# Performance work log

Hardware: AMD Instinct MI355X
Metric: run time of the kernel (lower is better)

## Reference

```python
import jax, jax.numpy as jnp
import numpy as np

EPS = 1e-12  # torch F.normalize clamp epsilon
NOISE = np.array([1e-05, 2e-05, 3e-05], dtype=np.float32)  # diagonal regularizer


def setup_inputs() -> dict:
    key = jax.random.key(0)
    B, C = 65536, 128
    v_feat = jax.random.normal(key, (B, C, 3), dtype=jnp.float32)
    return {"v_feat": v_feat}


def reference(v_feat):
    # L2 normalize each 3-vector (B, C, 3) along last dim
    norm = jnp.sqrt(jnp.sum(v_feat * v_feat, axis=-1, keepdims=True))
    v = v_feat / jnp.maximum(norm, EPS)

    # Covariance M = v^T v  -> (B, 3, 3), plus tiny diagonal noise for stability
    M = jnp.einsum('bci,bcj->bij', v, v) + jnp.diag(jnp.asarray(NOISE))[None, :, :]

    # Batched symmetric 3x3 eigendecomposition (ascending eigenvalues)
    _, evecs = jnp.linalg.eigh(M)  # evecs: (B, 3, 3), columns are eigenvectors
    v1 = evecs[:, :, 0]  # (B, 3)
    v2 = evecs[:, :, 1]

    # Sign disambiguation: align with the mean direction of the features
    def fix_sign(vec):
        s = jnp.sign(jnp.sum(v * vec[:, None, :], axis=(1, 2)))  # (B,)
        s = jnp.where(s == 0, 1.0, s)
        return vec * s[:, None]

    v1 = fix_sign(v1)
    v2 = fix_sign(v2)
    v3 = jnp.cross(v1, v2)

    # Frame: columns [v1 v2 v3] -> (B, 3, 3)
    return jnp.stack([v1, v2, v3], axis=-1)
```

## Files before the change

### kernel.cpp

```cpp
#include <hip/hip_runtime.h>
#include <math.h>
#include <stdint.h>


#define WAVES_PER_BLOCK 4
#define BLOCK (WAVES_PER_BLOCK * 64)
#define ITERS 2
#define BATCHES_PER_WAVE (4 * ITERS)
#define BPB (WAVES_PER_BLOCK * BATCHES_PER_WAVE)

template <int CTRL>
__device__ __forceinline__ float ror16_f32(float v) {
    union { float f; int i; } u, r;
    u.f = v;
    r.i = __builtin_amdgcn_mov_dpp(u.i, CTRL, 0xF, 0xF, true);
    return r.f;
}

__device__ __forceinline__ double fast_rsqrt2(double x) {
    double r = (double)__builtin_amdgcn_rsqf((float)x);
    double h = -0.5 * x;
    r = r * fma(h, r * r, 1.5);
    r = r * fma(h, r * r, 1.5);
    return r;
}
__device__ __forceinline__ double fast_rcp(double x) {
    double r = (double)__builtin_amdgcn_rcpf((float)x);
    r = r * fma(-x, r, 2.0);
    r = r * fma(-x, r, 2.0);
    return r;
}

template <int P, int Q, int R>
__device__ __forceinline__ void jrot(double (&A)[3][3], double (&V)[3][3]) {
    double apq = A[P][Q];
    if (fabs(apq) > 1e-18) {
        double theta = (A[Q][Q] - A[P][P]) * 0.5 * fast_rcp(apq);
        double q = fma(theta, theta, 1.0);
        double sq = (q < 1e37) ? q * fast_rsqrt2(q) : fabs(theta);
        double t = fast_rcp(fabs(theta) + sq);
        if (theta < 0.0) t = -t;
        double c = fast_rsqrt2(fma(t, t, 1.0));
        double s = t * c;
        double apq_t = t * apq;
        A[P][P] = A[P][P] - apq_t;
        A[Q][Q] = A[Q][Q] + apq_t;
        A[P][Q] = 0.0;
        A[Q][P] = 0.0;
        double apr = A[P][R], aqr = A[Q][R];
        A[P][R] = c * apr - s * aqr; A[R][P] = A[P][R];
        A[Q][R] = s * apr + c * aqr; A[R][Q] = A[Q][R];
#pragma unroll
        for (int i = 0; i < 3; ++i) {
            double vip = V[i][P], viq = V[i][Q];
            V[i][P] = c * vip - s * viq;
            V[i][Q] = s * vip + c * viq;
        }
    }
}

__global__ __launch_bounds__(BLOCK) void vn_fused(
    const float* __restrict__ vf, float* __restrict__ out, int B) {
    __shared__ float sA[BPB][9];

    const int tid  = threadIdx.x;
    const int wave = tid >> 6;
    const int lane = tid & 63;
    const int g    = lane >> 4;
    const int sub  = lane & 15;

    const int blockBase = blockIdx.x * BPB;

#pragma unroll
    for (int it = 0; it < ITERS; ++it) {
        const int bslot = wave * BATCHES_PER_WAVE + it * 4 + g;
        const int b = blockBase + bslot;
        if (b < B) {
            const float4* p4 =
                reinterpret_cast<const float4*>(vf + (size_t)b * 384 + sub * 24);
            float f[24];
#pragma unroll
            for (int i = 0; i < 6; ++i) {
                float4 q = p4[i];
                f[4 * i + 0] = q.x; f[4 * i + 1] = q.y;
                f[4 * i + 2] = q.z; f[4 * i + 3] = q.w;
            }

            float m[9];
#pragma unroll
            for (int k = 0; k < 9; ++k) m[k] = 0.0f;

#pragma unroll
            for (int k = 0; k < 8; ++k) {
                float fx = f[3 * k + 0];
                float fy = f[3 * k + 1];
                float fz = f[3 * k + 2];
                float n2 = fmaf(fx, fx, fmaf(fy, fy, fz * fz));
                float r = __builtin_amdgcn_rsqf(n2);
                r = r * fmaf(-0.5f * n2, r * r, 1.5f);
                float inv = (n2 > 1e-24f) ? r : 1e12f;
                float x = fx * inv;
                float y = fy * inv;
                float z = fz * inv;
                m[0] = fmaf(x, x, m[0]);
                m[1] = fmaf(x, y, m[1]);
                m[2] = fmaf(x, z, m[2]);
                m[3] = fmaf(y, y, m[3]);
                m[4] = fmaf(y, z, m[4]);
                m[5] = fmaf(z, z, m[5]);
                m[6] += x; m[7] += y; m[8] += z;
            }

#pragma unroll
            for (int k = 0; k < 9; ++k) m[k] += ror16_f32<0x121>(m[k]);
#pragma unroll
            for (int k = 0; k < 9; ++k) m[k] += ror16_f32<0x122>(m[k]);
#pragma unroll
            for (int k = 0; k < 9; ++k) m[k] += ror16_f32<0x124>(m[k]);
#pragma unroll
            for (int k = 0; k < 9; ++k) m[k] += ror16_f32<0x128>(m[k]);

            if (sub == 0) {
#pragma unroll
                for (int k = 0; k < 9; ++k) sA[bslot][k] = m[k];
            }
        }
    }

    __syncthreads();

    if (tid < BPB) {
        const int b = blockBase + tid;
        if (b < B) {
            double m[9];
#pragma unroll
            for (int k = 0; k < 9; ++k) m[k] = (double)sA[tid][k];

            double A[3][3], V[3][3];
            A[0][0] = m[0] + (double)1e-05f;
            A[0][1] = m[1]; A[1][0] = m[1];
            A[0][2] = m[2]; A[2][0] = m[2];
            A[1][1] = m[3] + (double)2e-05f;
            A[1][2] = m[4]; A[2][1] = m[4];
            A[2][2] = m[5] + (double)3e-05f;
#pragma unroll
            for (int i = 0; i < 3; ++i)
#pragma unroll
                for (int j = 0; j < 3; ++j) V[i][j] = (i == j) ? 1.0 : 0.0;

#pragma unroll
            for (int sweep = 0; sweep < 6; ++sweep) {
                jrot<0, 1, 2>(A, V);
                jrot<0, 2, 1>(A, V);
                jrot<1, 2, 0>(A, V);
            }

            double e0 = A[0][0], e1 = A[1][1], e2 = A[2][2];
            double c0x = V[0][0], c0y = V[1][0], c0z = V[2][0];
            double c1x = V[0][1], c1y = V[1][1], c1z = V[2][1];
            double c2x = V[0][2], c2y = V[1][2], c2z = V[2][2];

#define CSWAP(ea, eb, ax, ay, az, bx, by, bz)                         \
            if (ea > eb) {                                            \
                double t_;                                            \
                t_ = ea; ea = eb; eb = t_;                            \
                t_ = ax; ax = bx; bx = t_;                            \
                t_ = ay; ay = by; by = t_;                            \
                t_ = az; az = bz; bz = t_;                            \
            }
            CSWAP(e0, e1, c0x, c0y, c0z, c1x, c1y, c1z)
            CSWAP(e1, e2, c1x, c1y, c1z, c2x, c2y, c2z)
            CSWAP(e0, e1, c0x, c0y, c0z, c1x, c1y, c1z)
#undef CSWAP

            double s0 = m[6], s1 = m[7], s2 = m[8];
            double d1 = s0 * c0x + s1 * c0y + s2 * c0z;
            double f1 = (d1 < 0.0) ? -1.0 : 1.0;
            c0x *= f1; c0y *= f1; c0z *= f1;
            double d2 = s0 * c1x + s1 * c1y + s2 * c1z;
            double f2 = (d2 < 0.0) ? -1.0 : 1.0;
            c1x *= f2; c1y *= f2; c1z *= f2;

            double v3x = c0y * c1z - c0z * c1y;
            double v3y = c0z * c1x - c0x * c1z;
            double v3z = c0x * c1y - c0y * c1x;

            float* o = out + (size_t)b * 9;
            o[0] = (float)c0x; o[1] = (float)c1x; o[2] = (float)v3x;
            o[3] = (float)c0y; o[4] = (float)c1y; o[5] = (float)v3y;
            o[6] = (float)c0z; o[7] = (float)c1z; o[8] = (float)v3z;
        }
    }
}

extern "C" void kernel_launch(void* const* d_in, const int* in_sizes, int n_in,
                              void* d_out, int out_size, void* d_ws, size_t ws_size,
                              hipStream_t stream) {
    const float* vf = (const float*)d_in[0];
    float* out = (float*)d_out;
    const int B = in_sizes[0] / 384;
    const int grid = (B + BPB - 1) / BPB;
    vn_fused<<<dim3(grid), dim3(BLOCK), 0, stream>>>(vf, out, B);
}
```

Before: 25.66 us.

## Split into reduction and full-occupancy eigensolve kernels via workspace

Measured after the change: 26.10 us. Within noise of the previous version (+1.7%).

```diff
diff --git a/kernel.cpp b/kernel.cpp
--- a/kernel.cpp
+++ b/kernel.cpp
@@ -3,11 +3,9 @@
 #include <stdint.h>
 
 
-#define WAVES_PER_BLOCK 4
-#define BLOCK (WAVES_PER_BLOCK * 64)
+#define BLOCK 256
 #define ITERS 2
-#define BATCHES_PER_WAVE (4 * ITERS)
-#define BPB (WAVES_PER_BLOCK * BATCHES_PER_WAVE)
+#define BPB   32
 
 template <int CTRL>
 __device__ __forceinline__ float ror16_f32(float v) {
@@ -29,6 +27,65 @@
     r = r * fma(-x, r, 2.0);
     r = r * fma(-x, r, 2.0);
     return r;
+}
+
+__global__ __launch_bounds__(BLOCK) void vn_phase1(
+    const float* __restrict__ vf, float* __restrict__ wsm, int B) {
+    const int tid  = threadIdx.x;
+    const int wave = tid >> 6;
+    const int lane = tid & 63;
+    const int g    = lane >> 4;
+    const int sub  = lane & 15;
+
+    const int blockBase = blockIdx.x * BPB;
+
+#pragma unroll
+    for (int it = 0; it < ITERS; ++it) {
+        const int bslot = wave * (4 * ITERS) + it * 4 + g;
+        const int b = blockBase + bslot;
+        if (b < B) {
+            const float* base = vf + (size_t)b * 384;
+
+            float m[9];
+#pragma unroll
+            for (int k = 0; k < 9; ++k) m[k] = 0.0f;
+
+#pragma unroll
+            for (int j = 0; j < 8; ++j) {
+                const float3 v =
+                    *reinterpret_cast<const float3*>(base + (16 * j + sub) * 3);
+                float fx = v.x, fy = v.y, fz = v.z;
+                float n2 = fmaf(fx, fx, fmaf(fy, fy, fz * fz));
+                float r = __builtin_amdgcn_rsqf(n2);
+                r = r * fmaf(-0.5f * n2, r * r, 1.5f);
+                float inv = (n2 > 1e-24f) ? r : 1e12f;
+                float x = fx * inv;
+                float y = fy * inv;
+                float z = fz * inv;
+                m[0] = fmaf(x, x, m[0]);
+                m[1] = fmaf(x, y, m[1]);
+                m[2] = fmaf(x, z, m[2]);
+                m[3] = fmaf(y, y, m[3]);
+                m[4] = fmaf(y, z, m[4]);
+                m[5] = fmaf(z, z, m[5]);
+                m[6] += x; m[7] += y; m[8] += z;
+            }
+
+#pragma unroll
+            for (int k = 0; k < 9; ++k) m[k] += ror16_f32<0x121>(m[k]);
+#pragma unroll
+            for (int k = 0; k < 9; ++k) m[k] += ror16_f32<0x122>(m[k]);
+#pragma unroll
+            for (int k = 0; k < 9; ++k) m[k] += ror16_f32<0x124>(m[k]);
+#pragma unroll
+            for (int k = 0; k < 9; ++k) m[k] += ror16_f32<0x128>(m[k]);
+
+            if (sub == 0) {
+#pragma unroll
+                for (int k = 0; k < 9; ++k) wsm[(size_t)k * B + b] = m[k];
+            }
+        }
+    }
 }
 
 template <int P, int Q, int R>
@@ -59,138 +116,68 @@
     }
 }
 
-__global__ __launch_bounds__(BLOCK) void vn_fused(
-    const float* __restrict__ vf, float* __restrict__ out, int B) {
-    __shared__ float sA[BPB][9];
+__global__ __launch_bounds__(256) void vn_phase2(
+    const float* __restrict__ wsm, float* __restrict__ out, int B) {
+    const int b = blockIdx.x * 256 + threadIdx.x;
+    if (b >= B) return;
 
-    const int tid  = threadIdx.x;
-    const int wave = tid >> 6;
-    const int lane = tid & 63;
-    const int g    = lane >> 4;
-    const int sub  = lane & 15;
+    double m[9];
+#pragma unroll
+    for (int k = 0; k < 9; ++k) m[k] = (double)wsm[(size_t)k * B + b];
 
-    const int blockBase = blockIdx.x * BPB;
+    double A[3][3], V[3][3];
+    A[0][0] = m[0] + (double)1e-05f;
+    A[0][1] = m[1]; A[1][0] = m[1];
+    A[0][2] = m[2]; A[2][0] = m[2];
+    A[1][1] = m[3] + (double)2e-05f;
+    A[1][2] = m[4]; A[2][1] = m[4];
+    A[2][2] = m[5] + (double)3e-05f;
+#pragma unroll
+    for (int i = 0; i < 3; ++i)
+#pragma unroll
+        for (int j = 0; j < 3; ++j) V[i][j] = (i == j) ? 1.0 : 0.0;
 
 #pragma unroll
-    for (int it = 0; it < ITERS; ++it) {
-        const int bslot = wave * BATCHES_PER_WAVE + it * 4 + g;
-        const int b = blockBase + bslot;
-        if (b < B) {
-            const float4* p4 =
-                reinterpret_cast<const float4*>(vf + (size_t)b * 384 + sub * 24);
-            float f[24];
-#pragma unroll
-            for (int i = 0; i < 6; ++i) {
-                float4 q = p4[i];
-                f[4 * i + 0] = q.x; f[4 * i + 1] = q.y;
-                f[4 * i + 2] = q.z; f[4 * i + 3] = q.w;
-            }
-
-            float m[9];
-#pragma unroll
-            for (int k = 0; k < 9; ++k) m[k] = 0.0f;
-
-#pragma unroll
-            for (int k = 0; k < 8; ++k) {
-                float fx = f[3 * k + 0];
-                float fy = f[3 * k + 1];
-                float fz = f[3 * k + 2];
-                float n2 = fmaf(fx, fx, fmaf(fy, fy, fz * fz));
-                float r = __builtin_amdgcn_rsqf(n2);
-                r = r * fmaf(-0.5f * n2, r * r, 1.5f);
-                float inv = (n2 > 1e-24f) ? r : 1e12f;
-                float x = fx * inv;
-                float y = fy * inv;
-                float z = fz * inv;
-                m[0] = fmaf(x, x, m[0]);
-                m[1] = fmaf(x, y, m[1]);
-                m[2] = fmaf(x, z, m[2]);
-                m[3] = fmaf(y, y, m[3]);
-                m[4] = fmaf(y, z, m[4]);
-                m[5] = fmaf(z, z, m[5]);
-                m[6] += x; m[7] += y; m[8] += z;
-            }
-
-#pragma unroll
-            for (int k = 0; k < 9; ++k) m[k] += ror16_f32<0x121>(m[k]);
-#pragma unroll
-            for (int k = 0; k < 9; ++k) m[k] += ror16_f32<0x122>(m[k]);
-#pragma unroll
-            for (int k = 0; k < 9; ++k) m[k] += ror16_f32<0x124>(m[k]);
-#pragma unroll
-            for (int k = 0; k < 9; ++k) m[k] += ror16_f32<0x128>(m[k]);
-
-            if (sub == 0) {
-#pragma unroll
-                for (int k = 0; k < 9; ++k) sA[bslot][k] = m[k];
-            }
-        }
+    for (int sweep = 0; sweep < 4; ++sweep) {
+        jrot<0, 1, 2>(A, V);
+        jrot<0, 2, 1>(A, V);
+        jrot<1, 2, 0>(A, V);
     }
 
-    __syncthreads();
-
-    if (tid < BPB) {
-        const int b = blockBase + tid;
-        if (b < B) {
-            double m[9];
-#pragma unroll
-            for (int k = 0; k < 9; ++k) m[k] = (double)sA[tid][k];
-
-            double A[3][3], V[3][3];
-            A[0][0] = m[0] + (double)1e-05f;
-            A[0][1] = m[1]; A[1][0] = m[1];
-            A[0][2] = m[2]; A[2][0] = m[2];
-            A[1][1] = m[3] + (double)2e-05f;
-            A[1][2] = m[4]; A[2][1] = m[4];
-            A[2][2] = m[5] + (double)3e-05f;
-#pragma unroll
-            for (int i = 0; i < 3; ++i)
-#pragma unroll
-                for (int j = 0; j < 3; ++j) V[i][j] = (i == j) ? 1.0 : 0.0;
-
-#pragma unroll
-            for (int sweep = 0; sweep < 6; ++sweep) {
-                jrot<0, 1, 2>(A, V);
-                jrot<0, 2, 1>(A, V);
-                jrot<1, 2, 0>(A, V);
-            }
-
-            double e0 = A[0][0], e1 = A[1][1], e2 = A[2][2];
-            double c0x = V[0][0], c0y = V[1][0], c0z = V[2][0];
-            double c1x = V[0][1], c1y = V[1][1], c1z = V[2][1];
-            double c2x = V[0][2], c2y = V[1][2], c2z = V[2][2];
+    double e0 = A[0][0], e1 = A[1][1], e2 = A[2][2];
+    double c0x = V[0][0], c0y = V[1][0], c0z = V[2][0];
+    double c1x = V[0][1], c1y = V[1][1], c1z = V[2][1];
+    double c2x = V[0][2], c2y = V[1][2], c2z = V[2][2];
 
 #define CSWAP(ea, eb, ax, ay, az, bx, by, bz)                         \
-            if (ea > eb) {                                            \
-                double t_;                                            \
-                t_ = ea; ea = eb; eb = t_;                            \
-                t_ = ax; ax = bx; bx = t_;                            \
-                t_ = ay; ay = by; by = t_;                            \
-                t_ = az; az = bz; bz = t_;                            \
-            }
-            CSWAP(e0, e1, c0x, c0y, c0z, c1x, c1y, c1z)
-            CSWAP(e1, e2, c1x, c1y, c1z, c2x, c2y, c2z)
-            CSWAP(e0, e1, c0x, c0y, c0z, c1x, c1y, c1z)
+    if (ea > eb) {                                                    \
+        double t_;                                                    \
+        t_ = ea; ea = eb; eb = t_;                                    \
+        t_ = ax; ax = bx; bx = t_;                                    \
+        t_ = ay; ay = by; by = t_;                                    \
+        t_ = az; az = bz; bz = t_;                                    \
+    }
+    CSWAP(e0, e1, c0x, c0y, c0z, c1x, c1y, c1z)
+    CSWAP(e1, e2, c1x, c1y, c1z, c2x, c2y, c2z)
+    CSWAP(e0, e1, c0x, c0y, c0z, c1x, c1y, c1z)
 #undef CSWAP
 
-            double s0 = m[6], s1 = m[7], s2 = m[8];
-            double d1 = s0 * c0x + s1 * c0y + s2 * c0z;
-            double f1 = (d1 < 0.0) ? -1.0 : 1.0;
-            c0x *= f1; c0y *= f1; c0z *= f1;
-            double d2 = s0 * c1x + s1 * c1y + s2 * c1z;
-            double f2 = (d2 < 0.0) ? -1.0 : 1.0;
-            c1x *= f2; c1y *= f2; c1z *= f2;
+    double s0 = m[6], s1 = m[7], s2 = m[8];
+    double d1 = s0 * c0x + s1 * c0y + s2 * c0z;
+    double f1 = (d1 < 0.0) ? -1.0 : 1.0;
+    c0x *= f1; c0y *= f1; c0z *= f1;
+    double d2 = s0 * c1x + s1 * c1y + s2 * c1z;
+    double f2 = (d2 < 0.0) ? -1.0 : 1.0;
+    c1x *= f2; c1y *= f2; c1z *= f2;
 
-            double v3x = c0y * c1z - c0z * c1y;
-            double v3y = c0z * c1x - c0x * c1z;
-            double v3z = c0x * c1y - c0y * c1x;
+    double v3x = c0y * c1z - c0z * c1y;
+    double v3y = c0z * c1x - c0x * c1z;
+    double v3z = c0x * c1y - c0y * c1x;
 
-            float* o = out + (size_t)b * 9;
-            o[0] = (float)c0x; o[1] = (float)c1x; o[2] = (float)v3x;
-            o[3] = (float)c0y; o[4] = (float)c1y; o[5] = (float)v3y;
-            o[6] = (float)c0z; o[7] = (float)c1z; o[8] = (float)v3z;
-        }
-    }
+    float* o = out + (size_t)b * 9;
+    o[0] = (float)c0x; o[1] = (float)c1x; o[2] = (float)v3x;
+    o[3] = (float)c0y; o[4] = (float)c1y; o[5] = (float)v3y;
+    o[6] = (float)c0z; o[7] = (float)c1z; o[8] = (float)v3z;
 }
 
 extern "C" void kernel_launch(void* const* d_in, const int* in_sizes, int n_in,
@@ -198,7 +185,10 @@
                               hipStream_t stream) {
     const float* vf = (const float*)d_in[0];
     float* out = (float*)d_out;
+    float* wsm = (float*)d_ws;
     const int B = in_sizes[0] / 384;
-    const int grid = (B + BPB - 1) / BPB;
-    vn_fused<<<dim3(grid), dim3(BLOCK), 0, stream>>>(vf, out, B);
+    const int grid1 = (B + BPB - 1) / BPB;
+    vn_phase1<<<dim3(grid1), dim3(BLOCK), 0, stream>>>(vf, wsm, B);
+    const int grid2 = (B + 255) / 256;
+    vn_phase2<<<dim3(grid2), dim3(256), 0, stream>>>(wsm, out, B);
 }
```

## Switch Jacobi eigensolver to fp32 and hoist both batch loads ahead of compute

Applied to the files above, without the earlier changes.

Result: faster. 24.09 us (-6.1%).

```diff
diff --git a/kernel.cpp b/kernel.cpp
--- a/kernel.cpp
+++ b/kernel.cpp
@@ -3,11 +3,8 @@
 #include <stdint.h>
 
 
-#define WAVES_PER_BLOCK 4
-#define BLOCK (WAVES_PER_BLOCK * 64)
-#define ITERS 2
-#define BATCHES_PER_WAVE (4 * ITERS)
-#define BPB (WAVES_PER_BLOCK * BATCHES_PER_WAVE)
+#define BLOCK 256
+#define BPB   32
 
 template <int CTRL>
 __device__ __forceinline__ float ror16_f32(float v) {
@@ -17,46 +14,80 @@
     return r.f;
 }
 
-__device__ __forceinline__ double fast_rsqrt2(double x) {
-    double r = (double)__builtin_amdgcn_rsqf((float)x);
-    double h = -0.5 * x;
-    r = r * fma(h, r * r, 1.5);
-    r = r * fma(h, r * r, 1.5);
-    return r;
-}
-__device__ __forceinline__ double fast_rcp(double x) {
-    double r = (double)__builtin_amdgcn_rcpf((float)x);
-    r = r * fma(-x, r, 2.0);
-    r = r * fma(-x, r, 2.0);
-    return r;
+__device__ __forceinline__ float frsqrt(float x) {
+    float r = __builtin_amdgcn_rsqf(x);
+    return r * fmaf(-0.5f * x, r * r, 1.5f);
+}
+__device__ __forceinline__ float frcp(float x) {
+    float r = __builtin_amdgcn_rcpf(x);
+    return r * fmaf(-x, r, 2.0f);
 }
 
 template <int P, int Q, int R>
-__device__ __forceinline__ void jrot(double (&A)[3][3], double (&V)[3][3]) {
-    double apq = A[P][Q];
-    if (fabs(apq) > 1e-18) {
-        double theta = (A[Q][Q] - A[P][P]) * 0.5 * fast_rcp(apq);
-        double q = fma(theta, theta, 1.0);
-        double sq = (q < 1e37) ? q * fast_rsqrt2(q) : fabs(theta);
-        double t = fast_rcp(fabs(theta) + sq);
-        if (theta < 0.0) t = -t;
-        double c = fast_rsqrt2(fma(t, t, 1.0));
-        double s = t * c;
-        double apq_t = t * apq;
+__device__ __forceinline__ void jrot(float (&A)[3][3], float (&V)[3][3]) {
+    float apq = A[P][Q];
+    if (fabsf(apq) > 1e-12f) {
+        float theta = (A[Q][Q] - A[P][P]) * 0.5f * frcp(apq);
+        float q = fmaf(theta, theta, 1.0f);
+        float sq = q * frsqrt(q);
+        float t = frcp(fabsf(theta) + sq);
+        if (theta < 0.0f) t = -t;
+        float c = frsqrt(fmaf(t, t, 1.0f));
+        float s = t * c;
+        float apq_t = t * apq;
         A[P][P] = A[P][P] - apq_t;
         A[Q][Q] = A[Q][Q] + apq_t;
-        A[P][Q] = 0.0;
-        A[Q][P] = 0.0;
-        double apr = A[P][R], aqr = A[Q][R];
-        A[P][R] = c * apr - s * aqr; A[R][P] = A[P][R];
-        A[Q][R] = s * apr + c * aqr; A[R][Q] = A[Q][R];
+        A[P][Q] = 0.0f;
+        A[Q][P] = 0.0f;
+        float apr = A[P][R], aqr = A[Q][R];
+        A[P][R] = fmaf(c, apr, -s * aqr); A[R][P] = A[P][R];
+        A[Q][R] = fmaf(s, apr,  c * aqr); A[R][Q] = A[Q][R];
 #pragma unroll
         for (int i = 0; i < 3; ++i) {
-            double vip = V[i][P], viq = V[i][Q];
-            V[i][P] = c * vip - s * viq;
-            V[i][Q] = s * vip + c * viq;
-        }
-    }
+            float vip = V[i][P], viq = V[i][Q];
+            V[i][P] = fmaf(c, vip, -s * viq);
+            V[i][Q] = fmaf(s, vip,  c * viq);
+        }
+    }
+}
+
+__device__ __forceinline__ void accum8(const float4 (&q)[6], float (&m)[9]) {
+    float f[24];
+#pragma unroll
+    for (int i = 0; i < 6; ++i) {
+        f[4 * i + 0] = q[i].x; f[4 * i + 1] = q[i].y;
+        f[4 * i + 2] = q[i].z; f[4 * i + 3] = q[i].w;
+    }
+#pragma unroll
+    for (int k = 0; k < 8; ++k) {
+        float fx = f[3 * k + 0];
+        float fy = f[3 * k + 1];
+        float fz = f[3 * k + 2];
+        float n2 = fmaf(fx, fx, fmaf(fy, fy, fz * fz));
+        float r = __builtin_amdgcn_rsqf(n2);
+        float inv = (n2 > 1e-24f) ? r : 1e12f;
+        float x = fx * inv;
+        float y = fy * inv;
+        float z = fz * inv;
+        m[0] = fmaf(x, x, m[0]);
+        m[1] = fmaf(x, y, m[1]);
+        m[2] = fmaf(x, z, m[2]);
+        m[3] = fmaf(y, y, m[3]);
+        m[4] = fmaf(y, z, m[4]);
+        m[5] = fmaf(z, z, m[5]);
+        m[6] += x; m[7] += y; m[8] += z;
+    }
+}
+
+__device__ __forceinline__ void reduce16(float (&m)[9]) {
+#pragma unroll
+    for (int k = 0; k < 9; ++k) m[k] += ror16_f32<0x121>(m[k]);
+#pragma unroll
+    for (int k = 0; k < 9; ++k) m[k] += ror16_f32<0x122>(m[k]);
+#pragma unroll
+    for (int k = 0; k < 9; ++k) m[k] += ror16_f32<0x124>(m[k]);
+#pragma unroll
+    for (int k = 0; k < 9; ++k) m[k] += ror16_f32<0x128>(m[k]);
 }
 
 __global__ __launch_bounds__(BLOCK) void vn_fused(
@@ -70,60 +101,45 @@
     const int sub  = lane & 15;
 
     const int blockBase = blockIdx.x * BPB;
-
-#pragma unroll
-    for (int it = 0; it < ITERS; ++it) {
-        const int bslot = wave * BATCHES_PER_WAVE + it * 4 + g;
-        const int b = blockBase + bslot;
-        if (b < B) {
-            const float4* p4 =
-                reinterpret_cast<const float4*>(vf + (size_t)b * 384 + sub * 24);
-            float f[24];
-#pragma unroll
-            for (int i = 0; i < 6; ++i) {
-                float4 q = p4[i];
-                f[4 * i + 0] = q.x; f[4 * i + 1] = q.y;
-                f[4 * i + 2] = q.z; f[4 * i + 3] = q.w;
-            }
-
-            float m[9];
-#pragma unroll
-            for (int k = 0; k < 9; ++k) m[k] = 0.0f;
-
-#pragma unroll
-            for (int k = 0; k < 8; ++k) {
-                float fx = f[3 * k + 0];
-                float fy = f[3 * k + 1];
-                float fz = f[3 * k + 2];
-                float n2 = fmaf(fx, fx, fmaf(fy, fy, fz * fz));
-                float r = __builtin_amdgcn_rsqf(n2);
-                r = r * fmaf(-0.5f * n2, r * r, 1.5f);
-                float inv = (n2 > 1e-24f) ? r : 1e12f;
-                float x = fx * inv;
-                float y = fy * inv;
-                float z = fz * inv;
-                m[0] = fmaf(x, x, m[0]);
-                m[1] = fmaf(x, y, m[1]);
-                m[2] = fmaf(x, z, m[2]);
-                m[3] = fmaf(y, y, m[3]);
-                m[4] = fmaf(y, z, m[4]);
-                m[5] = fmaf(z, z, m[5]);
-                m[6] += x; m[7] += y; m[8] += z;
-            }
-
-#pragma unroll
-            for (int k = 0; k < 9; ++k) m[k] += ror16_f32<0x121>(m[k]);
-#pragma unroll
-            for (int k = 0; k < 9; ++k) m[k] += ror16_f32<0x122>(m[k]);
-#pragma unroll
-            for (int k = 0; k < 9; ++k) m[k] += ror16_f32<0x124>(m[k]);
-#pragma unroll
-            for (int k = 0; k < 9; ++k) m[k] += ror16_f32<0x128>(m[k]);
-
-            if (sub == 0) {
-#pragma unroll
-                for (int k = 0; k < 9; ++k) sA[bslot][k] = m[k];
-            }
+    const int slotA = wave * 8 + g;
+    const int slotB = wave * 8 + 4 + g;
+    const int bA = blockBase + slotA;
+    const int bB = blockBase + slotB;
+
+    float4 qa[6], qb[6];
+    if (bA < B) {
+        const float4* pa =
+            reinterpret_cast<const float4*>(vf + (size_t)bA * 384 + sub * 24);
+#pragma unroll
+        for (int i = 0; i < 6; ++i) qa[i] = pa[i];
+    }
+    if (bB < B) {
+        const float4* pb =
+            reinterpret_cast<const float4*>(vf + (size_t)bB * 384 + sub * 24);
+#pragma unroll
+        for (int i = 0; i < 6; ++i) qb[i] = pb[i];
+    }
+
+    if (bA < B) {
+        float m[9];
+#pragma unroll
+        for (int k = 0; k < 9; ++k) m[k] = 0.0f;
+        accum8(qa, m);
+        reduce16(m);
+        if (sub == 0) {
+#pragma unroll
+            for (int k = 0; k < 9; ++k) sA[slotA][k] = m[k];
+        }
+    }
+    if (bB < B) {
+        float m[9];
+#pragma unroll
+        for (int k = 0; k < 9; ++k) m[k] = 0.0f;
+        accum8(qb, m);
+        reduce16(m);
+        if (sub == 0) {
+#pragma unroll
+            for (int k = 0; k < 9; ++k) sA[slotB][k] = m[k];
         }
     }
 
@@ -132,21 +148,21 @@
     if (tid < BPB) {
         const int b = blockBase + tid;
         if (b < B) {
-            double m[9];
-#pragma unroll
-            for (int k = 0; k < 9; ++k) m[k] = (double)sA[tid][k];
-
-            double A[3][3], V[3][3];
-            A[0][0] = m[0] + (double)1e-05f;
+            float m[9];
+#pragma unroll
+            for (int k = 0; k < 9; ++k) m[k] = sA[tid][k];
+
+            float A[3][3], V[3][3];
+            A[0][0] = m[0] + 1e-05f;
             A[0][1] = m[1]; A[1][0] = m[1];
             A[0][2] = m[2]; A[2][0] = m[2];
-            A[1][1] = m[3] + (double)2e-05f;
+            A[1][1] = m[3] + 2e-05f;
             A[1][2] = m[4]; A[2][1] = m[4];
-            A[2][2] = m[5] + (double)3e-05f;
+            A[2][2] = m[5] + 3e-05f;
 #pragma unroll
             for (int i = 0; i < 3; ++i)
 #pragma unroll
-                for (int j = 0; j < 3; ++j) V[i][j] = (i == j) ? 1.0 : 0.0;
+                for (int j = 0; j < 3; ++j) V[i][j] = (i == j) ? 1.0f : 0.0f;
 
 #pragma unroll
             for (int sweep = 0; sweep < 6; ++sweep) {
@@ -155,14 +171,14 @@
                 jrot<1, 2, 0>(A, V);
             }
 
-            double e0 = A[0][0], e1 = A[1][1], e2 = A[2][2];
-            double c0x = V[0][0], c0y = V[1][0], c0z = V[2][0];
-            double c1x = V[0][1], c1y = V[1][1], c1z = V[2][1];
-            double c2x = V[0][2], c2y = V[1][2], c2z = V[2][2];
+            float e0 = A[0][0], e1 = A[1][1], e2 = A[2][2];
+            float c0x = V[0][0], c0y = V[1][0], c0z = V[2][0];
+            float c1x = V[0][1], c1y = V[1][1], c1z = V[2][1];
+            float c2x = V[0][2], c2y = V[1][2], c2z = V[2][2];
 
 #define CSWAP(ea, eb, ax, ay, az, bx, by, bz)                         \
             if (ea > eb) {                                            \
-                double t_;                                            \
+                float t_;                                             \
                 t_ = ea; ea = eb; eb = t_;                            \
                 t_ = ax; ax = bx; bx = t_;                            \
                 t_ = ay; ay = by; by = t_;                            \
@@ -173,22 +189,22 @@
             CSWAP(e0, e1, c0x, c0y, c0z, c1x, c1y, c1z)
 #undef CSWAP
 
-            double s0 = m[6], s1 = m[7], s2 = m[8];
-            double d1 = s0 * c0x + s1 * c0y + s2 * c0z;
-            double f1 = (d1 < 0.0) ? -1.0 : 1.0;
+            float s0 = m[6], s1 = m[7], s2 = m[8];
+            float d1 = s0 * c0x + s1 * c0y + s2 * c0z;
+            float f1 = (d1 < 0.0f) ? -1.0f : 1.0f;
             c0x *= f1; c0y *= f1; c0z *= f1;
-            double d2 = s0 * c1x + s1 * c1y + s2 * c1z;
-            double f2 = (d2 < 0.0) ? -1.0 : 1.0;
+            float d2 = s0 * c1x + s1 * c1y + s2 * c1z;
+            float f2 = (d2 < 0.0f) ? -1.0f : 1.0f;
             c1x *= f2; c1y *= f2; c1z *= f2;
 
-            double v3x = c0y * c1z - c0z * c1y;
-            double v3y = c0z * c1x - c0x * c1z;
-            double v3z = c0x * c1y - c0y * c1x;
+            float v3x = c0y * c1z - c0z * c1y;
+            float v3y = c0z * c1x - c0x * c1z;
+            float v3z = c0x * c1y - c0y * c1x;
 
             float* o = out + (size_t)b * 9;
-            o[0] = (float)c0x; o[1] = (float)c1x; o[2] = (float)v3x;
-            o[3] = (float)c0y; o[4] = (float)c1y; o[5] = (float)v3y;
-            o[6] = (float)c0z; o[7] = (float)c1z; o[8] = (float)v3z;
+            o[0] = c0x; o[1] = c1x; o[2] = v3x;
+            o[3] = c0y; o[4] = c1y; o[5] = v3y;
+            o[6] = c0z; o[7] = c1z; o[8] = v3z;
         }
     }
 }
```
